# Performance work log

Measured on AMD Instinct MI355X. Metric: run time of the kernel, lower is better.

## Reference

```python
import jax, jax.numpy as jnp
import numpy as np

B, OBS, H, A, E = 131072, 194, 64, 5, 3  # batch, obs dim, hidden, max_action_dim, n event types


def setup_inputs() -> dict:
    key = jax.random.key(0)
    ks = jax.random.split(key, 16)
    s = lambda k, shape, std=0.1: (jax.random.normal(k, shape, dtype=jnp.float32) * std)
    return {
        "x": jax.random.normal(ks[0], (B, OBS), dtype=jnp.float32),
        "action": jax.random.randint(ks[1], (B,), 0, A),
        "W1": s(ks[2], (OBS, H)), "b1": jnp.zeros((H,), jnp.float32),
        "W2": s(ks[3], (H, H)),   "b2": jnp.zeros((H,), jnp.float32),
        "Wh": s(ks[4], (E, H, A), 0.01), "bh": jnp.zeros((E, A), jnp.float32),
        "Wc1": s(ks[5], (OBS, H)), "bc1": jnp.zeros((H,), jnp.float32),
        "Wc2": s(ks[6], (H, H)),   "bc2": jnp.zeros((H,), jnp.float32),
        "Wc3": s(ks[7], (H, 1)),   "bc3": jnp.zeros((1,), jnp.float32),
    }


def reference(x, action, W1, b1, W2, b2, Wh, bh, Wc1, bc1, Wc2, bc2, Wc3, bc3):
    # shared trunk
    feat = jnp.tanh(jnp.tanh(x @ W1 + b1) @ W2 + b2)          # [B, H]
    # route each sample to one of E heads via argmax of first 3 obs dims
    ev = jnp.argmax(x[:, :E], axis=1)                          # [B] int
    all_logits = jnp.einsum('bh,eha->bea', feat, Wh) + bh      # [B, E, A]
    logits = jnp.take_along_axis(
        all_logits, jnp.broadcast_to(ev[:, None, None], (x.shape[0], 1, A)), axis=1
    )[:, 0]                                                    # [B, A]
    logp_all = jax.nn.log_softmax(logits, axis=-1)             # [B, A]
    logp = jnp.take_along_axis(logp_all, action[:, None], axis=1)[:, 0]  # [B]
    entropy = -jnp.sum(jnp.exp(logp_all) * logp_all, axis=-1)  # [B]
    # critic
    value = jnp.tanh(jnp.tanh(x @ Wc1 + bc1) @ Wc2 + bc2) @ Wc3 + bc3    # [B, 1]
    return action, logp, entropy, value
```

## Files before the change

### kernel.cpp

```cpp
#include <hip/hip_runtime.h>
#include <hip/hip_bf16.h>

constexpr int Bt    = 131072;
constexpr int OBS   = 194;

constexpr int W1B_S  = 0;
constexpr int WC1B_S = 14336;
constexpr int W2B_S  = 28672;
constexpr int WC2B_S = 36864;
constexpr int WHB_S  = 45056;
constexpr size_t EVG_B = 98304;
constexpr size_t HG_S  = 131072;

typedef short bf8   __attribute__((ext_vector_type(8)));
typedef float f32x4 __attribute__((ext_vector_type(4)));
typedef unsigned int u32;

__device__ __forceinline__ short f2bs(float f) {
    union { __hip_bfloat16 h; short s; } u;
    u.h = __float2bfloat16(f);
    return u.s;
}
__device__ __forceinline__ float bs2f(short s) {
    union { short s; __hip_bfloat16 h; } u;
    u.s = s;
    return __bfloat162float(u.h);
}
__device__ __forceinline__ u32 pk2(float a, float b) {
    union { __hip_bfloat162 h; u32 u; } r;
    r.h = __float22bfloat162_rn(float2{a, b});
    return r.u;
}
__device__ __forceinline__ float fast_tanh(float v) {
    v = fminf(fmaxf(v, -15.f), 15.f);
    float e = __expf(2.f * v);
    return (e - 1.f) * __builtin_amdgcn_rcpf(e + 1.f);
}
__device__ __forceinline__ void dma16(const void* g, void* s) {
    __builtin_amdgcn_global_load_lds(
        (const __attribute__((address_space(1))) u32*)g,
        (__attribute__((address_space(3))) u32*)s, 16, 0, 0);
}

__global__ void __launch_bounds__(256) prep(
    const float* __restrict__ W1, const float* __restrict__ b1,
    const float* __restrict__ W2, const float* __restrict__ Wh,
    const float* __restrict__ Wc1, const float* __restrict__ bc1,
    const float* __restrict__ Wc2, const float* __restrict__ Wc3,
    short* __restrict__ ws)
{
    const int gid = blockIdx.x * 256 + threadIdx.x;
    const int gsz = gridDim.x * 256;

    for (int i = gid; i < 14336; i += gsz) {
        int j = i & 7, l = (i >> 3) & 63, nt = (i >> 9) & 3, kb = i >> 11;
        int k = kb * 32 + ((l >> 4) << 3) + j;
        int n = nt * 16 + (l & 15);
        short v1 = 0, v2 = 0;
        if (k < OBS) {
            v1 = f2bs(W1[k * 64 + n]);
            v2 = f2bs(Wc1[k * 64 + n]);
        } else if (k == OBS) {
            v1 = f2bs(b1[n]);
            v2 = f2bs(bc1[n]);
        }
        ws[W1B_S + i]  = v1;
        ws[WC1B_S + i] = v2;
    }
    for (int i = gid; i < 8192; i += gsz) {
        int j = i & 7, l = (i >> 3) & 63, nt = (i >> 9) & 3, kb = i >> 11;
        int s = kb * 32 + ((l >> 4) << 3) + j;
        int kp = (s & 3) * 16 + (s >> 2);
        int n = nt * 16 + (l & 15);
        ws[W2B_S + i]  = f2bs(W2[kp * 64 + n]);
        ws[WC2B_S + i] = f2bs(Wc2[kp * 64 + n]);
    }
    for (int i = gid; i < 1024; i += gsz) {
        int j = i & 7, l = (i >> 3) & 63, kb = i >> 9;
        int s = kb * 32 + ((l >> 4) << 3) + j;
        int kp = (s & 3) * 16 + (s >> 2);
        int cc = l & 15;
        float v;
        if (cc == 15) v = Wc3[kp];
        else { int e = cc / 5, a = cc - 5 * e; v = Wh[(e * 64 + kp) * 5 + a]; }
        ws[WHB_S + i] = f2bs(v);
    }
}

constexpr int P1_XS0 = 57344;
constexpr int P1_XSS = 12544;
constexpr int P1_LDS = P1_XS0 + 8 * P1_XSS;

__global__ void __launch_bounds__(512, 2) trunk1(
    const float* __restrict__ x, const short* __restrict__ ws,
    short* __restrict__ hG, unsigned char* __restrict__ evG)
{
    __shared__ __align__(16) char smem[P1_LDS];
    const int t = threadIdx.x;
    const int w = t >> 6, l = t & 63, q = l >> 4, c = l & 15;

    #pragma unroll
    for (int i = 0; i < 7; ++i) {
        int idx = i * 512 + t;
        dma16((const char*)ws + idx * 16, smem + idx * 16);
    }

    char* xs = smem + P1_XS0 + w * P1_XSS;
    const int t0 = blockIdx.x * 32 + w * 4;

    {
        const char* src = (const char*)x + (size_t)t0 * 12416;
        #pragma unroll
        for (int ch = 0; ch < 12; ++ch)
            dma16(src + ch * 1024 + l * 16, xs + ch * 1024 + l * 16);
        if (l < 8) {
            int4 v = *reinterpret_cast<const int4*>(src + 12288 + l * 16);
            *reinterpret_cast<int4*>(xs + 12288 + l * 16) = v;
        }
    }

    __syncthreads();

    const bf8* fW1L  = reinterpret_cast<const bf8*>(smem);
    const bf8* fWc1L = reinterpret_cast<const bf8*>(smem + 28672);
    short* ha = reinterpret_cast<short*>(xs);
    short* hc = ha + 1152;

    #pragma unroll 1
    for (int i = 0; i < 4; ++i) {
        const int tt = t0 + i;

        asm volatile("s_waitcnt vmcnt(0)" ::: "memory");
        __builtin_amdgcn_sched_barrier(0);

        union AF { u32 u[4]; bf8 v; } af[7];
        #pragma unroll
        for (int kb = 0; kb < 6; ++kb) {
            #pragma unroll
            for (int j = 0; j < 4; ++j) {
                float2 v = *reinterpret_cast<const float2*>(xs + c * 776 + kb * 128 + q * 32 + j * 8);
                af[kb].u[j] = pk2(v.x, v.y);
            }
        }
        af[6].u[0] = 0; af[6].u[1] = 0; af[6].u[2] = 0; af[6].u[3] = 0;
        if (q == 0) {
            float2 v = *reinterpret_cast<const float2*>(xs + c * 776 + 768);
            af[6].u[0] = pk2(v.x, v.y);
            af[6].u[1] = pk2(1.0f, 0.0f);
        }
        if (l < 16) {
            float2 v01 = *reinterpret_cast<const float2*>(xs + l * 776);
            float  v2  = *reinterpret_cast<const float*>(xs + l * 776 + 8);
            int ev = 0; float b = v01.x;
            if (v01.y > b) { b = v01.y; ev = 1; }
            if (v2 > b) ev = 2;
            evG[tt * 16 + l] = (unsigned char)ev;
        }

        f32x4 aa[4], ac[4];
        #pragma unroll
        for (int nt = 0; nt < 4; ++nt) {
            aa[nt] = f32x4{0.f, 0.f, 0.f, 0.f};
            ac[nt] = f32x4{0.f, 0.f, 0.f, 0.f};
        }
        #pragma unroll
        for (int kb = 0; kb < 7; ++kb) {
            bf8 a = af[kb].v;
            #pragma unroll
            for (int nt = 0; nt < 4; ++nt) {
                aa[nt] = __builtin_amdgcn_mfma_f32_16x16x32_bf16(a, fW1L [(kb * 4 + nt) * 64 + l], aa[nt], 0, 0, 0);
                ac[nt] = __builtin_amdgcn_mfma_f32_16x16x32_bf16(a, fWc1L[(kb * 4 + nt) * 64 + l], ac[nt], 0, 0, 0);
            }
        }
        #pragma unroll
        for (int r = 0; r < 4; ++r) {
            uint2 pa, pc;
            pa.x = pk2(fast_tanh(aa[0][r]), fast_tanh(aa[1][r]));
            pa.y = pk2(fast_tanh(aa[2][r]), fast_tanh(aa[3][r]));
            pc.x = pk2(fast_tanh(ac[0][r]), fast_tanh(ac[1][r]));
            pc.y = pk2(fast_tanh(ac[2][r]), fast_tanh(ac[3][r]));
            *reinterpret_cast<uint2*>(&ha[(q * 4 + r) * 72 + 4 * c]) = pa;
            *reinterpret_cast<uint2*>(&hc[(q * 4 + r) * 72 + 4 * c]) = pc;
        }
        #pragma unroll
        for (int kb = 0; kb < 2; ++kb) {
            bf8 va = *reinterpret_cast<const bf8*>(&ha[c * 72 + kb * 32 + q * 8]);
            bf8 vc = *reinterpret_cast<const bf8*>(&hc[c * 72 + kb * 32 + q * 8]);
            *reinterpret_cast<bf8*>(hG + ((size_t)(tt * 4 + kb)     * 64 + l) * 8) = va;
            *reinterpret_cast<bf8*>(hG + ((size_t)(tt * 4 + 2 + kb) * 64 + l) * 8) = vc;
        }

        if (i < 3) {
            const char* src = (const char*)x + (size_t)(tt + 1) * 12416;
            #pragma unroll
            for (int ch = 0; ch < 12; ++ch)
                dma16(src + ch * 1024 + l * 16, xs + ch * 1024 + l * 16);
            if (l < 8) {
                int4 v = *reinterpret_cast<const int4*>(src + 12288 + l * 16);
                *reinterpret_cast<int4*>(xs + 12288 + l * 16) = v;
            }
        }
    }
}

constexpr int F2_W   = 34816;
constexpr int F2_PW  = 5248;
constexpr int F2_LDS = F2_W + 8 * F2_PW;

__global__ void __launch_bounds__(512, 4) head2(
    const int* __restrict__ act_in,
    const float* __restrict__ b2, const float* __restrict__ bc2,
    const float* __restrict__ bh, const float* __restrict__ bc3,
    const short* __restrict__ ws,
    const short* __restrict__ hG, const unsigned char* __restrict__ evG,
    float* __restrict__ out)
{
    __shared__ __align__(16) char smem[F2_LDS];
    const int t = threadIdx.x;
    const int w = t >> 6, l = t & 63, q = l >> 4, c = l & 15;

    #pragma unroll
    for (int i = 0; i < 5; ++i) {
        int idx = i * 512 + t;
        if (idx < 2176)
            dma16((const char*)ws + 57344 + idx * 16, smem + idx * 16);
    }

    float b2v[4], bc2v[4];
    #pragma unroll
    for (int nt = 0; nt < 4; ++nt) {
        b2v[nt]  = b2[nt * 16 + c];
        bc2v[nt] = bc2[nt * 16 + c];
    }
    float bhv = (c < 15) ? bh[c] : bc3[0];

    __syncthreads();

    const bf8* fW2L  = reinterpret_cast<const bf8*>(smem);
    const bf8* fWc2L = reinterpret_cast<const bf8*>(smem + 16384);
    const bf8* fWhL  = reinterpret_cast<const bf8*>(smem + 32768);
    short* ha = reinterpret_cast<short*>(smem + F2_W + w * F2_PW);
    short* hc = ha + 1152;
    short* lw = reinterpret_cast<short*>(smem + F2_W + w * F2_PW + 4608);
    float* vb = reinterpret_cast<float*>(smem + F2_W + w * F2_PW + 5184);

    #pragma unroll 1
    for (int i = 0; i < 2; ++i) {
        const int tt = blockIdx.x * 16 + w * 2 + i;
        const int gm = tt * 16 + c;
        int act = 0, evc = 0;
        if (l < 16) { act = act_in[gm]; evc = evG[gm]; }

        bf8 xa[2], xc[2];
        #pragma unroll
        for (int kb = 0; kb < 2; ++kb) {
            xa[kb] = *reinterpret_cast<const bf8*>(hG + ((size_t)(tt * 4 + kb)     * 64 + l) * 8);
            xc[kb] = *reinterpret_cast<const bf8*>(hG + ((size_t)(tt * 4 + 2 + kb) * 64 + l) * 8);
        }

        f32x4 aa[4], ac[4];
        #pragma unroll
        for (int nt = 0; nt < 4; ++nt) {
            aa[nt] = f32x4{b2v[nt], b2v[nt], b2v[nt], b2v[nt]};
            ac[nt] = f32x4{bc2v[nt], bc2v[nt], bc2v[nt], bc2v[nt]};
        }
        #pragma unroll
        for (int kb = 0; kb < 2; ++kb) {
            #pragma unroll
            for (int nt = 0; nt < 4; ++nt) {
                aa[nt] = __builtin_amdgcn_mfma_f32_16x16x32_bf16(xa[kb], fW2L [(kb * 4 + nt) * 64 + l], aa[nt], 0, 0, 0);
                ac[nt] = __builtin_amdgcn_mfma_f32_16x16x32_bf16(xc[kb], fWc2L[(kb * 4 + nt) * 64 + l], ac[nt], 0, 0, 0);
            }
        }
        #pragma unroll
        for (int r = 0; r < 4; ++r) {
            uint2 pa, pc;
            pa.x = pk2(fast_tanh(aa[0][r]), fast_tanh(aa[1][r]));
            pa.y = pk2(fast_tanh(aa[2][r]), fast_tanh(aa[3][r]));
            pc.x = pk2(fast_tanh(ac[0][r]), fast_tanh(ac[1][r]));
            pc.y = pk2(fast_tanh(ac[2][r]), fast_tanh(ac[3][r]));
            *reinterpret_cast<uint2*>(&ha[(q * 4 + r) * 72 + 4 * c]) = pa;
            *reinterpret_cast<uint2*>(&hc[(q * 4 + r) * 72 + 4 * c]) = pc;
        }

        {
            f32x4 lg = f32x4{bhv, bhv, bhv, bhv};
            f32x4 vv = f32x4{bhv, bhv, bhv, bhv};
            #pragma unroll
            for (int kb = 0; kb < 2; ++kb) {
                bf8 bw = fWhL[kb * 64 + l];
                bf8 fa = *reinterpret_cast<const bf8*>(&ha[c * 72 + kb * 32 + q * 8]);
                bf8 fc = *reinterpret_cast<const bf8*>(&hc[c * 72 + kb * 32 + q * 8]);
                lg = __builtin_amdgcn_mfma_f32_16x16x32_bf16(fa, bw, lg, 0, 0, 0);
                vv = __builtin_amdgcn_mfma_f32_16x16x32_bf16(fc, bw, vv, 0, 0, 0);
            }
            #pragma unroll
            for (int r = 0; r < 4; ++r)
                lw[(q * 4 + r) * 18 + c] = f2bs(lg[r]);
            if (c == 15) {
                #pragma unroll
                for (int r = 0; r < 4; ++r)
                    vb[q * 4 + r] = vv[r];
            }
        }

        if (l < 16) {
            float lg[5];
            #pragma unroll
            for (int a = 0; a < 5; ++a)
                lg[a] = bs2f(lw[c * 18 + evc * 5 + a]);
            float mx = lg[0];
            #pragma unroll
            for (int a = 1; a < 5; ++a) mx = fmaxf(mx, lg[a]);
            float se = 0.f;
            #pragma unroll
            for (int a = 0; a < 5; ++a) se += __expf(lg[a] - mx);
            float lse = __logf(se) + mx;
            float lsel = lg[0];
            #pragma unroll
            for (int a = 1; a < 5; ++a) lsel = (act == a) ? lg[a] : lsel;
            float ent = 0.f;
            #pragma unroll
            for (int a = 0; a < 5; ++a) { float lp = lg[a] - lse; ent -= __expf(lp) * lp; }

            out[gm]          = (float)act;
            out[Bt + gm]     = lsel - lse;
            out[2 * Bt + gm] = ent;
            out[3 * Bt + gm] = vb[c];
        }
    }
}

extern "C" void kernel_launch(void* const* d_in, const int* in_sizes, int n_in,
                              void* d_out, int out_size, void* d_ws, size_t ws_size,
                              hipStream_t stream) {
    const float* x   = (const float*)d_in[0];
    const int*   act = (const int*)  d_in[1];
    const float* W1  = (const float*)d_in[2];
    const float* b1  = (const float*)d_in[3];
    const float* W2  = (const float*)d_in[4];
    const float* b2  = (const float*)d_in[5];
    const float* Wh  = (const float*)d_in[6];
    const float* bh  = (const float*)d_in[7];
    const float* Wc1 = (const float*)d_in[8];
    const float* bc1 = (const float*)d_in[9];
    const float* Wc2 = (const float*)d_in[10];
    const float* bc2 = (const float*)d_in[11];
    const float* Wc3 = (const float*)d_in[12];
    const float* bc3 = (const float*)d_in[13];
    float* out = (float*)d_out;
    short* ws  = (short*)d_ws;
    short* hG  = ws + HG_S;
    unsigned char* evG = (unsigned char*)d_ws + EVG_B;

    hipLaunchKernelGGL(prep, dim3(32), dim3(256), 0, stream,
                       W1, b1, W2, Wh, Wc1, bc1, Wc2, Wc3, ws);
    hipLaunchKernelGGL(trunk1, dim3(256), dim3(512), 0, stream,
                       x, ws, hG, evG);
    hipLaunchKernelGGL(head2, dim3(512), dim3(512), 0, stream,
                       act, b2, bc2, bh, bc3, ws, hG, evG, out);
}
```

Measured before the change: 200.7 us.

## Prefetch next x tile before MFMAs and move hidden transpose into head kernel

The trunk kernel now issues the async DMA for the next x tile right after reading the current tile into registers, so the load overlaps the layer-1 MFMAs. Previously it was issued only at the end of each iteration. The tail of each tile is now staged with one overlapping DMA in place of a register copy. The trunk writes tanh outputs straight to global in row layout, and the LDS transpose moves into the head kernel. This gives the trunk less LDS traffic and fewer syncs, but the head kernel takes on the LDS round-trip and uses narrower 8-byte global accesses.

```diff
diff --git a/kernel.cpp b/kernel.cpp
--- a/kernel.cpp
+++ b/kernel.cpp
@@ -108,30 +108,28 @@
     char* xs = smem + P1_XS0 + w * P1_XSS;
     const int t0 = blockIdx.x * 32 + w * 4;
 
-    {
-        const char* src = (const char*)x + (size_t)t0 * 12416;
+    auto stage = [&](int tt) {
+        const char* src = (const char*)x + (size_t)tt * 12416;
         #pragma unroll
         for (int ch = 0; ch < 12; ++ch)
             dma16(src + ch * 1024 + l * 16, xs + ch * 1024 + l * 16);
-        if (l < 8) {
-            int4 v = *reinterpret_cast<const int4*>(src + 12288 + l * 16);
-            *reinterpret_cast<int4*>(xs + 12288 + l * 16) = v;
-        }
-    }
+        dma16(src + 11392 + l * 16, xs + 11392 + l * 16);
+    };
+    stage(t0);
 
     __syncthreads();
 
     const bf8* fW1L  = reinterpret_cast<const bf8*>(smem);
     const bf8* fWc1L = reinterpret_cast<const bf8*>(smem + 28672);
-    short* ha = reinterpret_cast<short*>(xs);
-    short* hc = ha + 1152;
 
     #pragma unroll 1
     for (int i = 0; i < 4; ++i) {
         const int tt = t0 + i;
 
-        asm volatile("s_waitcnt vmcnt(0)" ::: "memory");
-        __builtin_amdgcn_sched_barrier(0);
+        if (i) {
+            asm volatile("s_waitcnt vmcnt(0)" ::: "memory");
+            __builtin_amdgcn_sched_barrier(0);
+        }
 
         union AF { u32 u[4]; bf8 v; } af[7];
         #pragma unroll
@@ -157,6 +155,10 @@
             evG[tt * 16 + l] = (unsigned char)ev;
         }
 
+        __builtin_amdgcn_sched_barrier(0);
+        if (i < 3) stage(tt + 1);
+        __builtin_amdgcn_sched_barrier(0);
+
         f32x4 aa[4], ac[4];
         #pragma unroll
         for (int nt = 0; nt < 4; ++nt) {
@@ -172,6 +174,7 @@
                 ac[nt] = __builtin_amdgcn_mfma_f32_16x16x32_bf16(a, fWc1L[(kb * 4 + nt) * 64 + l], ac[nt], 0, 0, 0);
             }
         }
+        short* hGt = hG + (size_t)tt * 2048;
         #pragma unroll
         for (int r = 0; r < 4; ++r) {
             uint2 pa, pc;
@@ -179,26 +182,8 @@
             pa.y = pk2(fast_tanh(aa[2][r]), fast_tanh(aa[3][r]));
             pc.x = pk2(fast_tanh(ac[0][r]), fast_tanh(ac[1][r]));
             pc.y = pk2(fast_tanh(ac[2][r]), fast_tanh(ac[3][r]));
-            *reinterpret_cast<uint2*>(&ha[(q * 4 + r) * 72 + 4 * c]) = pa;
-            *reinterpret_cast<uint2*>(&hc[(q * 4 + r) * 72 + 4 * c]) = pc;
-        }
-        #pragma unroll
-        for (int kb = 0; kb < 2; ++kb) {
-            bf8 va = *reinterpret_cast<const bf8*>(&ha[c * 72 + kb * 32 + q * 8]);
-            bf8 vc = *reinterpret_cast<const bf8*>(&hc[c * 72 + kb * 32 + q * 8]);
-            *reinterpret_cast<bf8*>(hG + ((size_t)(tt * 4 + kb)     * 64 + l) * 8) = va;
-            *reinterpret_cast<bf8*>(hG + ((size_t)(tt * 4 + 2 + kb) * 64 + l) * 8) = vc;
-        }
-
-        if (i < 3) {
-            const char* src = (const char*)x + (size_t)(tt + 1) * 12416;
-            #pragma unroll
-            for (int ch = 0; ch < 12; ++ch)
-                dma16(src + ch * 1024 + l * 16, xs + ch * 1024 + l * 16);
-            if (l < 8) {
-                int4 v = *reinterpret_cast<const int4*>(src + 12288 + l * 16);
-                *reinterpret_cast<int4*>(xs + 12288 + l * 16) = v;
-            }
+            *reinterpret_cast<uint2*>(hGt + (q * 4 + r) * 64 + 4 * c)        = pa;
+            *reinterpret_cast<uint2*>(hGt + 1024 + (q * 4 + r) * 64 + 4 * c) = pc;
         }
     }
 }
@@ -251,11 +236,23 @@
         int act = 0, evc = 0;
         if (l < 16) { act = act_in[gm]; evc = evG[gm]; }
 
+        const short* hGt = hG + (size_t)tt * 2048;
+        uint2 va[4], vc2[4];
+        #pragma unroll
+        for (int r = 0; r < 4; ++r) {
+            va[r]  = *reinterpret_cast<const uint2*>(hGt + (q * 4 + r) * 64 + 4 * c);
+            vc2[r] = *reinterpret_cast<const uint2*>(hGt + 1024 + (q * 4 + r) * 64 + 4 * c);
+        }
+        #pragma unroll
+        for (int r = 0; r < 4; ++r) {
+            *reinterpret_cast<uint2*>(&ha[(q * 4 + r) * 72 + 4 * c]) = va[r];
+            *reinterpret_cast<uint2*>(&hc[(q * 4 + r) * 72 + 4 * c]) = vc2[r];
+        }
         bf8 xa[2], xc[2];
         #pragma unroll
         for (int kb = 0; kb < 2; ++kb) {
-            xa[kb] = *reinterpret_cast<const bf8*>(hG + ((size_t)(tt * 4 + kb)     * 64 + l) * 8);
-            xc[kb] = *reinterpret_cast<const bf8*>(hG + ((size_t)(tt * 4 + 2 + kb) * 64 + l) * 8);
+            xa[kb] = *reinterpret_cast<const bf8*>(&ha[c * 72 + kb * 32 + q * 8]);
+            xc[kb] = *reinterpret_cast<const bf8*>(&hc[c * 72 + kb * 32 + q * 8]);
         }
 
         f32x4 aa[4], ac[4];
```

Measured after the change: 197.8 us. Within noise of the previous version (-1.4%).
